# Kernel tuning notes

Hardware: AMD Instinct MI355X
Metric: run time of the kernel (lower is better)

The kernel has to match this reference:

```python
import jax, jax.numpy as jnp
import numpy as np

N = 50000
E = 400000
IN_FEATS = 512
HEADS = 8
OUT_FEATS = 64
NEG_SLOPE = 0.2


def setup_inputs() -> dict:
    key = jax.random.key(0)
    ks = jax.random.split(key, 12)
    HF = HEADS * OUT_FEATS
    s = 1.0 / np.sqrt(IN_FEATS)
    inp = {
        "feat": jax.random.normal(ks[0], (N, IN_FEATS), dtype=jnp.float32),
        "src": jax.random.randint(ks[1], (E,), 0, N, dtype=jnp.int32),
        "dst": jax.random.randint(ks[2], (E,), 0, N, dtype=jnp.int32),
        "W_src": jax.random.normal(ks[3], (IN_FEATS, HF), dtype=jnp.float32) * s,
        "b_src": jax.random.normal(ks[4], (HF,), dtype=jnp.float32) * 0.01,
        "W_dst": jax.random.normal(ks[5], (IN_FEATS, HF), dtype=jnp.float32) * s,
        "b_dst": jax.random.normal(ks[6], (HF,), dtype=jnp.float32) * 0.01,
        "W_val": jax.random.normal(ks[7], (IN_FEATS, HF), dtype=jnp.float32) * s,
        "b_val": jax.random.normal(ks[8], (HF,), dtype=jnp.float32) * 0.01,
        "attn_l": jax.random.normal(ks[9], (HEADS, OUT_FEATS), dtype=jnp.float32) * 0.1,
        "attn_r": jax.random.normal(ks[10], (HEADS, OUT_FEATS), dtype=jnp.float32) * 0.1,
    }
    return inp


def reference(feat, src, dst, W_src, b_src, W_dst, b_dst, W_val, b_val, attn_l, attn_r):
    # node projections: [N, H, F]
    feat_src = (feat @ W_src + b_src).reshape(N, HEADS, OUT_FEATS)
    feat_dst = (feat @ W_dst + b_dst).reshape(N, HEADS, OUT_FEATS)
    feat_v = (feat @ W_val + b_val).reshape(N, HEADS, OUT_FEATS)

    # per-node attention logits: [N, H]
    el = jnp.einsum("nhf,hf->nh", feat_src, attn_l)
    er = jnp.einsum("nhf,hf->nh", feat_dst, attn_r)

    # per-edge logits with leaky relu: [E, H]
    e = el[src] + er[dst]
    e = jnp.where(e >= 0, e, NEG_SLOPE * e)

    # edge softmax segmented by destination node
    e_max = jax.ops.segment_max(e, dst, num_segments=N)  # [N, H]
    e_max = jnp.where(jnp.isfinite(e_max), e_max, 0.0)
    exp_e = jnp.exp(e - e_max[dst])  # [E, H]
    denom = jax.ops.segment_sum(exp_e, dst, num_segments=N)  # [N, H]
    a = exp_e / jnp.maximum(denom[dst], 1e-16)  # [E, H]

    # weighted gather-scatter aggregation: [N, H, F]
    msg = feat_v[src] * a[:, :, None]
    rst = jax.ops.segment_sum(msg, dst, num_segments=N)
    return rst.reshape(N, HEADS * OUT_FEATS)
```

## Files before the change

kernel.cpp:

```cpp
#include <hip/hip_runtime.h>
#include <math.h>

constexpr int N_NODES = 50000;
constexpr int N_PAD   = 50048;
constexpr int N_EDGES = 400000;
constexpr int IN_F = 512;
constexpr int HEADS = 8;
constexpr int OUT_F = 64;
constexpr int HF = 512;
constexpr float NEG = 0.2f;

typedef __bf16 bf16x8 __attribute__((ext_vector_type(8)));
typedef float  f32x4  __attribute__((ext_vector_type(4)));

__device__ __forceinline__ unsigned short f2bf(float f) {
    unsigned u = __float_as_uint(f);
    u += 0x7fffu + ((u >> 16) & 1u);
    return (unsigned short)(u >> 16);
}
__device__ __forceinline__ unsigned packbf2(float lo, float hi) {
    return (unsigned)f2bf(lo) | ((unsigned)f2bf(hi) << 16);
}

constexpr int K14_HIST0 = 289;
constexpr int K14_BLOCKS = K14_HIST0 + (N_EDGES + 255) / 256;

__global__ __launch_bounds__(256) void k14_misc(
        const float* __restrict__ W_val, unsigned short* __restrict__ Wt,
        const float* __restrict__ W_src, const float* __restrict__ b_src,
        const float* __restrict__ W_dst, const float* __restrict__ b_dst,
        const float* __restrict__ attn_l, const float* __restrict__ attn_r,
        unsigned short* __restrict__ w_lr, float* __restrict__ c_lr,
        const int* __restrict__ dst, int* __restrict__ deg) {
    __shared__ float tile[32][33];
    int b = blockIdx.x, t = threadIdx.x;
    if (b < 256) {
        int bi = b >> 4, bj = b & 15;
        for (int i = t; i < 1024; i += 256) {
            int r = i >> 5, c = i & 31;
            tile[r][c] = W_val[(size_t)(bi * 32 + r) * HF + bj * 32 + c];
        }
        __syncthreads();
        for (int i = t; i < 1024; i += 256) {
            int r = i >> 5, c = i & 31;
            Wt[(size_t)(bj * 32 + r) * IN_F + bi * 32 + c] = f2bf(tile[c][r]);
        }
    } else if (b < K14_HIST0) {
        int gid = (b - 256) * 256 + t;
        if (gid < 4096) {
            int k = gid >> 3, h = gid & 7;
            float s = 0.f;
            #pragma unroll 8
            for (int f = 0; f < OUT_F; ++f) s += W_src[k * HF + h * OUT_F + f] * attn_l[h * OUT_F + f];
            w_lr[h * IN_F + k] = f2bf(s);
        } else if (gid < 8192) {
            int g = gid - 4096;
            int k = g >> 3, h = g & 7;
            float s = 0.f;
            #pragma unroll 8
            for (int f = 0; f < OUT_F; ++f) s += W_dst[k * HF + h * OUT_F + f] * attn_r[h * OUT_F + f];
            w_lr[(8 + h) * IN_F + k] = f2bf(s);
        } else if (gid < 8192 + 16) {
            int g = gid - 8192;
            int h = g & 7;
            float s = 0.f;
            if (g < 8) {
                for (int f = 0; f < OUT_F; ++f) s += b_src[h * OUT_F + f] * attn_l[h * OUT_F + f];
                c_lr[h] = s;
            } else {
                for (int f = 0; f < OUT_F; ++f) s += b_dst[h * OUT_F + f] * attn_r[h * OUT_F + f];
                c_lr[8 + h] = s;
            }
        }
    } else {
        int e = (b - K14_HIST0) * 256 + t;
        if (e < N_EDGES) atomicAdd(&deg[dst[e]], 1);
    }
}

__global__ __launch_bounds__(1024) void kS_scan(const int* __restrict__ deg,
                                                int* __restrict__ offs,
                                                int* __restrict__ cursor) {
    __shared__ int wsum[16];
    __shared__ int base_s;
    int b = blockIdx.x, t = threadIdx.x;
    int lane = t & 63, wid = t >> 6;

    int pre = 0;
    for (int i = t; i < b * 1024; i += 1024) pre += deg[i];
    #pragma unroll
    for (int off = 32; off; off >>= 1) pre += __shfl_down(pre, (unsigned)off, 64);
    if (lane == 0) wsum[wid] = pre;
    __syncthreads();
    if (t == 0) {
        int s = 0;
        for (int i = 0; i < 16; ++i) s += wsum[i];
        base_s = s;
    }
    __syncthreads();
    int base = base_s;
    __syncthreads();

    int i = b * 1024 + t;
    int v = (i < N_NODES) ? deg[i] : 0;
    int x = v;
    #pragma unroll
    for (int off = 1; off < 64; off <<= 1) {
        int y = __shfl_up(x, (unsigned)off, 64);
        if (lane >= off) x += y;
    }
    if (lane == 63) wsum[wid] = x;
    __syncthreads();
    if (wid == 0) {
        int s = (lane < 16) ? wsum[lane] : 0;
        #pragma unroll
        for (int off = 1; off < 16; off <<= 1) {
            int y = __shfl_up(s, (unsigned)off, 64);
            if (lane >= off) s += y;
        }
        if (lane < 16) wsum[lane] = s;
    }
    __syncthreads();
    int woff = wid ? wsum[wid - 1] : 0;
    if (i < N_NODES) {
        int excl = base + woff + x - v;
        offs[i] = excl;
        cursor[i] = excl;
    }
}

constexpr int K3_GEMM = 8 * 49 * 4;
constexpr int K36_BLOCKS = K3_GEMM + (N_EDGES + 255) / 256;

__global__ __launch_bounds__(256) void k36_gemm_scatter(
        const float* __restrict__ feat,
        const unsigned short* __restrict__ Bbf,
        const unsigned short* __restrict__ w_lr,
        const float* __restrict__ c_lr,
        const float* __restrict__ bias,
        unsigned short* __restrict__ C,
        float* __restrict__ el, float* __restrict__ er,
        const int* __restrict__ src, const int* __restrict__ dst,
        int* __restrict__ cursor, int* __restrict__ srcs) {
    __shared__ unsigned short As[2][128 * 64];
    __shared__ unsigned short Bs[2][128 * 64];

    int b = blockIdx.x;
    if (b >= K3_GEMM) {
        int e = (b - K3_GEMM) * 256 + threadIdx.x;
        if (e < N_EDGES) {
            int pos = atomicAdd(&cursor[dst[e]], 1);
            srcs[pos] = src[e];
        }
        return;
    }

    int xcd = b & 7;
    int r0 = b >> 3;
    int bn = r0 & 3;
    int bm = xcd + 8 * (r0 >> 2);
    if (bm >= N_PAD / 128) return;

    int tid = threadIdx.x;
    int w = tid >> 6, lane = tid & 63;
    int rowBase = bm * 128, colBase = bn * 128;
    int wm = w >> 1, wn = w & 1;
    int c15 = lane & 15, q = lane >> 4;
    bool doE = (bn == 0) && (wn == 0);

    f32x4 acc[4][4] = {};
    f32x4 accE[4] = {};

    int e0 = w * 256 + lane;
    float4 pa[4], pb[4];

    auto LOADA = [&](int k0) {
        #pragma unroll
        for (int rnd = 0; rnd < 4; ++rnd) {
            int e = e0 + rnd * 64;
            int r = e >> 3, p = e & 7;
            int lc = p ^ (r & 7);
            int row = rowBase + r;
            if (row > N_NODES - 1) row = N_NODES - 1;
            const float* g = feat + (size_t)row * IN_F + k0 + lc * 8;
            pa[rnd] = *(const float4*)g;
            pb[rnd] = *(const float4*)(g + 4);
        }
    };
    auto ISSUEB = [&](int k0, int buf) {
        #pragma unroll
        for (int rnd = 0; rnd < 4; ++rnd) {
            int e = e0 + rnd * 64;
            int r = e >> 3, p = e & 7;
            int lc = p ^ (r & 7);
            const unsigned short* g = Bbf + (size_t)(colBase + r) * IN_F + k0 + lc * 8;
            __builtin_amdgcn_global_load_lds(
                (const __attribute__((address_space(1))) unsigned int*)g,
                (__attribute__((address_space(3))) unsigned int*)&Bs[buf][e * 8],
                16, 0, 0);
        }
    };
    auto WRITEA = [&](int buf) {
        #pragma unroll
        for (int rnd = 0; rnd < 4; ++rnd) {
            int e = e0 + rnd * 64;
            uint4 pk;
            pk.x = packbf2(pa[rnd].x, pa[rnd].y);
            pk.y = packbf2(pa[rnd].z, pa[rnd].w);
            pk.z = packbf2(pb[rnd].x, pb[rnd].y);
            pk.w = packbf2(pb[rnd].z, pb[rnd].w);
            *(uint4*)&As[buf][e * 8] = pk;
        }
    };

    LOADA(0);
    ISSUEB(0, 0);
    WRITEA(0);
    __syncthreads();

    for (int k0 = 0; k0 < IN_F; k0 += 64) {
        int cur = (k0 >> 6) & 1, nxt = cur ^ 1;
        bool more = (k0 + 64) < IN_F;
        if (more) { LOADA(k0 + 64); ISSUEB(k0 + 64, nxt); }

        #pragma unroll
        for (int ks = 0; ks < 2; ++ks) {
            bf16x8 a[4], bb[4];
            #pragma unroll
            for (int mi = 0; mi < 4; ++mi) {
                int row = wm * 64 + mi * 16 + c15;
                int pc = (ks * 4 + q) ^ (row & 7);
                a[mi] = *(const bf16x8*)&As[cur][row * 64 + pc * 8];
            }
            #pragma unroll
            for (int nj = 0; nj < 4; ++nj) {
                int row = wn * 64 + nj * 16 + c15;
                int pc = (ks * 4 + q) ^ (row & 7);
                bb[nj] = *(const bf16x8*)&Bs[cur][row * 64 + pc * 8];
            }
            #pragma unroll
            for (int mi = 0; mi < 4; ++mi)
                #pragma unroll
                for (int nj = 0; nj < 4; ++nj)
                    acc[mi][nj] = __builtin_amdgcn_mfma_f32_16x16x32_bf16(
                        a[mi], bb[nj], acc[mi][nj], 0, 0, 0);
            if (doE) {
                bf16x8 be = *(const bf16x8*)(w_lr + (size_t)c15 * IN_F + k0 + ks * 32 + q * 8);
                #pragma unroll
                for (int mi = 0; mi < 4; ++mi)
                    accE[mi] = __builtin_amdgcn_mfma_f32_16x16x32_bf16(
                        a[mi], be, accE[mi], 0, 0, 0);
            }
        }

        if (more) WRITEA(nxt);
        __syncthreads();
    }

    #pragma unroll
    for (int nj = 0; nj < 4; ++nj) {
        int col = colBase + wn * 64 + nj * 16 + c15;
        float bv = bias[col];
        #pragma unroll
        for (int mi = 0; mi < 4; ++mi) {
            int row0 = rowBase + wm * 64 + mi * 16 + q * 4;
            #pragma unroll
            for (int rg = 0; rg < 4; ++rg) {
                C[(size_t)(row0 + rg) * HF + col] = f2bf(acc[mi][nj][rg] + bv);
            }
        }
    }

    if (doE) {
        float cadd = c_lr[c15];
        int side = c15 >> 3, hh = c15 & 7;
        #pragma unroll
        for (int mi = 0; mi < 4; ++mi) {
            int row0 = rowBase + wm * 64 + mi * 16 + q * 4;
            #pragma unroll
            for (int rg = 0; rg < 4; ++rg) {
                float v = accE[mi][rg] + cadd;
                if (side) er[(size_t)(row0 + rg) * 8 + hh] = v;
                else      el[(size_t)(row0 + rg) * 8 + hh] = v;
            }
        }
    }
}

__device__ __forceinline__ void accum8(float* acc, uint4 v, float w) {
    unsigned u;
    u = v.x;
    acc[0] = fmaf(w, __uint_as_float(u << 16), acc[0]);
    acc[1] = fmaf(w, __uint_as_float(u & 0xffff0000u), acc[1]);
    u = v.y;
    acc[2] = fmaf(w, __uint_as_float(u << 16), acc[2]);
    acc[3] = fmaf(w, __uint_as_float(u & 0xffff0000u), acc[3]);
    u = v.z;
    acc[4] = fmaf(w, __uint_as_float(u << 16), acc[4]);
    acc[5] = fmaf(w, __uint_as_float(u & 0xffff0000u), acc[5]);
    u = v.w;
    acc[6] = fmaf(w, __uint_as_float(u << 16), acc[6]);
    acc[7] = fmaf(w, __uint_as_float(u & 0xffff0000u), acc[7]);
}

__global__ __launch_bounds__(256) void k8_agg(
        const int* __restrict__ srcs, const int* __restrict__ offs,
        const int* __restrict__ deg,
        const float* __restrict__ el, const float* __restrict__ er,
        const uint4* __restrict__ feat_v,
        float* __restrict__ out) {
    int lane = threadIdx.x & 63;
    int n = blockIdx.x * 4 + (threadIdx.x >> 6);
    int start = offs[n], cnt = deg[n];
    int h = lane >> 3;
    float erh = er[(size_t)n * 8 + h];
    float acc[8] = {};
    float dsum = 0.f;

    for (int base = 0; base < cnt; base += 64) {
        int m = cnt - base; if (m > 64) m = 64;
        int s_all = (lane < m) ? srcs[start + base + lane] : 0;
        int i = 0;
        for (; i + 8 <= m; i += 8) {
            int s[8]; uint4 v[8]; float e[8];
            #pragma unroll
            for (int j = 0; j < 8; ++j) s[j] = __shfl(s_all, i + j, 64);
            #pragma unroll
            for (int j = 0; j < 8; ++j) v[j] = feat_v[(size_t)s[j] * 64 + lane];
            #pragma unroll
            for (int j = 0; j < 8; ++j) e[j] = el[(size_t)s[j] * 8 + h];
            #pragma unroll
            for (int j = 0; j < 8; ++j) {
                float x = e[j] + erh;
                x = (x >= 0.f) ? x : NEG * x;
                float w = __expf(x);
                dsum += w;
                accum8(acc, v[j], w);
            }
        }
        for (; i < m; ++i) {
            int s0 = __shfl(s_all, i, 64);
            uint4 v0 = feat_v[(size_t)s0 * 64 + lane];
            float x = el[(size_t)s0 * 8 + h] + erh;
            x = (x >= 0.f) ? x : NEG * x;
            float w = __expf(x);
            dsum += w;
            accum8(acc, v0, w);
        }
    }

    float dn = 1.f / fmaxf(dsum, 1e-16f);
    float* op = out + (size_t)n * HF + lane * 8;
    *(float4*)op       = make_float4(acc[0] * dn, acc[1] * dn, acc[2] * dn, acc[3] * dn);
    *(float4*)(op + 4) = make_float4(acc[4] * dn, acc[5] * dn, acc[6] * dn, acc[7] * dn);
}

extern "C" void kernel_launch(void* const* d_in, const int* in_sizes, int n_in,
                              void* d_out, int out_size, void* d_ws, size_t ws_size,
                              hipStream_t stream) {
    const float* feat   = (const float*)d_in[0];
    const int*   src    = (const int*)d_in[1];
    const int*   dst    = (const int*)d_in[2];
    const float* W_src  = (const float*)d_in[3];
    const float* b_src  = (const float*)d_in[4];
    const float* W_dst  = (const float*)d_in[5];
    const float* b_dst  = (const float*)d_in[6];
    const float* W_val  = (const float*)d_in[7];
    const float* b_val  = (const float*)d_in[8];
    const float* attn_l = (const float*)d_in[9];
    const float* attn_r = (const float*)d_in[10];
    float* out = (float*)d_out;

    char* ws = (char*)d_ws;
    size_t off = 0;
    auto alloc = [&](size_t bytes) -> void* {
        void* p = ws + off;
        off += (bytes + 255) & ~(size_t)255;
        return p;
    };

    unsigned short* Wt      = (unsigned short*)alloc((size_t)IN_F * HF * 2);
    unsigned short* feat_v  = (unsigned short*)alloc((size_t)N_PAD * HF * 2);
    unsigned short* w_lr    = (unsigned short*)alloc((size_t)16 * IN_F * 2);
    float* c_lr   = (float*)alloc(16 * 4);
    float* el     = (float*)alloc((size_t)N_PAD * 8 * 4);
    float* er     = (float*)alloc((size_t)N_PAD * 8 * 4);
    int*   deg    = (int*)alloc((size_t)N_NODES * 4);
    int*   offs   = (int*)alloc((size_t)N_NODES * 4);
    int*   cursor = (int*)alloc((size_t)N_NODES * 4);
    int*   srcs   = (int*)alloc((size_t)N_EDGES * 4);
    (void)ws_size; (void)in_sizes; (void)n_in; (void)out_size;

    hipMemsetAsync(deg, 0, (size_t)N_NODES * 4, stream);
    k14_misc<<<K14_BLOCKS, 256, 0, stream>>>(W_val, Wt, W_src, b_src, W_dst, b_dst,
                                             attn_l, attn_r, w_lr, c_lr, dst, deg);
    kS_scan<<<(N_NODES + 1023) / 1024, 1024, 0, stream>>>(deg, offs, cursor);
    k36_gemm_scatter<<<K36_BLOCKS, 256, 0, stream>>>(feat, Wt, w_lr, c_lr, b_val,
                                                     feat_v, el, er,
                                                     src, dst, cursor, srcs);
    k8_agg<<<N_NODES / 4, 256, 0, stream>>>(srcs, offs, deg, el, er,
                                            (const uint4*)feat_v, out);
}
```

Measured before the change: 355.3 us.

## Load A operand directly from global into MFMA registers, drop LDS staging

The GEMM no longer stages the fp32 feature tile through shared memory. Each wave now loads its A fragments straight from global memory and converts them to bf16 in registers. This removes the LDS writes and reads for A and halves shared-memory use, which may allow more blocks per CU. The cost is that the two wn-waves sharing a row block now each fetch the same A data from global/L2. The loads are also no longer prefetched one k-step ahead, so global latency sits directly in front of the MFMAs.

```diff
diff --git a/kernel.cpp b/kernel.cpp
--- a/kernel.cpp
+++ b/kernel.cpp
@@ -142,7 +142,6 @@
         float* __restrict__ el, float* __restrict__ er,
         const int* __restrict__ src, const int* __restrict__ dst,
         int* __restrict__ cursor, int* __restrict__ srcs) {
-    __shared__ unsigned short As[2][128 * 64];
     __shared__ unsigned short Bs[2][128 * 64];
 
     int b = blockIdx.x;
@@ -168,25 +167,18 @@
     int c15 = lane & 15, q = lane >> 4;
     bool doE = (bn == 0) && (wn == 0);
 
+    const float* aptr[4];
+    #pragma unroll
+    for (int mi = 0; mi < 4; ++mi) {
+        int r = rowBase + wm * 64 + mi * 16 + c15;
+        if (r > N_NODES - 1) r = N_NODES - 1;
+        aptr[mi] = feat + (size_t)r * IN_F;
+    }
+
     f32x4 acc[4][4] = {};
     f32x4 accE[4] = {};
-
     int e0 = w * 256 + lane;
-    float4 pa[4], pb[4];
-
-    auto LOADA = [&](int k0) {
-        #pragma unroll
-        for (int rnd = 0; rnd < 4; ++rnd) {
-            int e = e0 + rnd * 64;
-            int r = e >> 3, p = e & 7;
-            int lc = p ^ (r & 7);
-            int row = rowBase + r;
-            if (row > N_NODES - 1) row = N_NODES - 1;
-            const float* g = feat + (size_t)row * IN_F + k0 + lc * 8;
-            pa[rnd] = *(const float4*)g;
-            pb[rnd] = *(const float4*)(g + 4);
-        }
-    };
+
     auto ISSUEB = [&](int k0, int buf) {
         #pragma unroll
         for (int rnd = 0; rnd < 4; ++rnd) {
@@ -200,37 +192,28 @@
                 16, 0, 0);
         }
     };
-    auto WRITEA = [&](int buf) {
-        #pragma unroll
-        for (int rnd = 0; rnd < 4; ++rnd) {
-            int e = e0 + rnd * 64;
-            uint4 pk;
-            pk.x = packbf2(pa[rnd].x, pa[rnd].y);
-            pk.y = packbf2(pa[rnd].z, pa[rnd].w);
-            pk.z = packbf2(pb[rnd].x, pb[rnd].y);
-            pk.w = packbf2(pb[rnd].z, pb[rnd].w);
-            *(uint4*)&As[buf][e * 8] = pk;
-        }
-    };
-
-    LOADA(0);
+
     ISSUEB(0, 0);
-    WRITEA(0);
     __syncthreads();
 
     for (int k0 = 0; k0 < IN_F; k0 += 64) {
         int cur = (k0 >> 6) & 1, nxt = cur ^ 1;
-        bool more = (k0 + 64) < IN_F;
-        if (more) { LOADA(k0 + 64); ISSUEB(k0 + 64, nxt); }
+        if (k0 + 64 < IN_F) ISSUEB(k0 + 64, nxt);
 
         #pragma unroll
         for (int ks = 0; ks < 2; ++ks) {
             bf16x8 a[4], bb[4];
             #pragma unroll
             for (int mi = 0; mi < 4; ++mi) {
-                int row = wm * 64 + mi * 16 + c15;
-                int pc = (ks * 4 + q) ^ (row & 7);
-                a[mi] = *(const bf16x8*)&As[cur][row * 64 + pc * 8];
+                const float* g = aptr[mi] + k0 + ks * 32 + q * 8;
+                float4 fa = *(const float4*)g;
+                float4 fb = *(const float4*)(g + 4);
+                bf16x8 t;
+                t[0] = (__bf16)fa.x; t[1] = (__bf16)fa.y;
+                t[2] = (__bf16)fa.z; t[3] = (__bf16)fa.w;
+                t[4] = (__bf16)fb.x; t[5] = (__bf16)fb.y;
+                t[6] = (__bf16)fb.z; t[7] = (__bf16)fb.w;
+                a[mi] = t;
             }
             #pragma unroll
             for (int nj = 0; nj < 4; ++nj) {
@@ -252,8 +235,6 @@
                         a[mi], be, accE[mi], 0, 0, 0);
             }
         }
-
-        if (more) WRITEA(nxt);
         __syncthreads();
     }
 
```

New measurement: 419.2 us. 18.0% more time.
